# Performance work log

Hardware: AMD Instinct MI355X
Metric: run time of the kernel (lower is better)

The kernel has to match this reference:

```python
import jax, jax.numpy as jnp
import numpy as np
from jax import lax


def _conv(x, w, b, padding):
    # x: NCHW, w: OIHW
    out = lax.conv_general_dilated(x, w, (1, 1), padding,
                                   dimension_numbers=('NCHW', 'OIHW', 'NCHW'))
    return out + b[None, :, None, None]


def _bilinear_sample(img, ys, xs):
    # img: [B,C,H,W]; ys, xs: [B,N] absolute pixel coords; zero padding outside.
    B, C, H, W = img.shape
    y0 = jnp.floor(ys); x0 = jnp.floor(xs)
    wy1 = ys - y0; wy0 = 1.0 - wy1
    wx1 = xs - x0; wx0 = 1.0 - wx1
    img_flat = img.reshape(B, C, H * W)

    def corner(yc, xc, w):
        valid = (yc >= 0) & (yc <= H - 1) & (xc >= 0) & (xc <= W - 1)
        yi = jnp.clip(yc, 0, H - 1).astype(jnp.int32)
        xi = jnp.clip(xc, 0, W - 1).astype(jnp.int32)
        idx = yi * W + xi  # [B,N]
        g = jax.vmap(lambda im, i: im[:, i])(img_flat, idx)  # [B,C,N]
        return g * (w * valid.astype(img.dtype))[:, None, :]

    return (corner(y0, x0, wy0 * wx0) + corner(y0, x0 + 1, wy0 * wx1)
            + corner(y0 + 1, x0, wy1 * wx0) + corner(y0 + 1, x0 + 1, wy1 * wx1))


def setup_inputs() -> dict:
    key = jax.random.key(0)
    ks = jax.random.split(key, 20)
    B, C, Co, H, W = 8, 64, 64, 128, 128
    f = jnp.float32

    def w_init(k, shape):
        fan_in = int(np.prod(shape[1:]))
        return jax.random.normal(k, shape, dtype=f) * (1.0 / np.sqrt(fan_in))

    inp = {
        'x': jax.random.normal(ks[0], (B, C, H, W), dtype=f),
        'offset': jax.random.normal(ks[1], (B, 18, H, W), dtype=f),
        # STN localization
        'stn_w1': w_init(ks[2], (32, C, 7, 7)), 'stn_b1': jnp.zeros((32,), f),
        'stn_w2': w_init(ks[3], (64, 32, 5, 5)), 'stn_b2': jnp.zeros((64,), f),
        'fc_w': jax.random.normal(ks[4], (6, 64), dtype=f) * 0.01,
        'fc_b': jnp.array([1, 0, 0, 0, 1, 0], f) + jax.random.normal(ks[5], (6,), dtype=f) * 0.02,
        # DeformConv2d
        'dcn_w': w_init(ks[6], (C, C, 3, 3)), 'dcn_b': jnp.zeros((C,), f),
        # weight_gen 1x1
        'wg_w': w_init(ks[7], (2, 2 * C, 1, 1)), 'wg_b': jnp.zeros((2,), f),
        # ELK block
        'w3': w_init(ks[8], (Co, C, 3, 3)), 'b3': jnp.zeros((Co,), f),
        'w15': w_init(ks[9], (Co, C, 1, 5)), 'b15': jnp.zeros((Co,), f),
        'w51': w_init(ks[10], (Co, C, 5, 1)), 'b51': jnp.zeros((Co,), f),
        'w1': w_init(ks[11], (Co, 3 * Co, 1, 1)), 'b1': jnp.zeros((Co,), f),
    }
    return inp


def _forward(x, offset, stn_w1, stn_b1, stn_w2, stn_b2, fc_w, fc_b,
             dcn_w, dcn_b, wg_w, wg_b, w3, b3, w15, b15, w51, b51, w1, b1):
    B, C, H, W = x.shape

    # ---- STN ----
    h = jax.nn.relu(_conv(x, stn_w1, stn_b1, [(3, 3), (3, 3)]))
    h = lax.reduce_window(h, -jnp.inf, lax.max, (1, 1, 2, 2), (1, 1, 2, 2), 'VALID')
    h = jax.nn.relu(_conv(h, stn_w2, stn_b2, [(2, 2), (2, 2)]))
    feat = h.mean(axis=(2, 3))  # AdaptiveAvgPool2d(1) -> [B,64]
    theta = (feat @ fc_w.T + fc_b).reshape(B, 2, 3)

    # affine_grid, align_corners=False
    xs_n = (2.0 * jnp.arange(W, dtype=x.dtype) + 1.0) / W - 1.0
    ys_n = (2.0 * jnp.arange(H, dtype=x.dtype) + 1.0) / H - 1.0
    Xn, Yn = jnp.meshgrid(xs_n, ys_n, indexing='xy')  # [H,W]
    gx = theta[:, 0, 0, None, None] * Xn + theta[:, 0, 1, None, None] * Yn + theta[:, 0, 2, None, None]
    gy = theta[:, 1, 0, None, None] * Xn + theta[:, 1, 1, None, None] * Yn + theta[:, 1, 2, None, None]
    # grid_sample unnormalize, align_corners=False
    ix = ((gx + 1.0) * W - 1.0) * 0.5
    iy = ((gy + 1.0) * H - 1.0) * 0.5
    Fs = _bilinear_sample(x, iy.reshape(B, -1), ix.reshape(B, -1)).reshape(B, C, H, W)

    # ---- DeformConv2d(k=3, pad=1): offset layout [.., 2k]=dy, [.., 2k+1]=dx ----
    off = offset.reshape(B, 9, 2, H, W)
    ki = (jnp.arange(9, dtype=x.dtype) // 3) - 1.0  # kernel dy
    kj = (jnp.arange(9, dtype=x.dtype) % 3) - 1.0   # kernel dx
    Yb = jnp.arange(H, dtype=x.dtype)[:, None]
    Xb = jnp.arange(W, dtype=x.dtype)[None, :]
    sy = Yb[None, None] + ki[None, :, None, None] + off[:, :, 0]  # [B,9,H,W]
    sx = Xb[None, None] + kj[None, :, None, None] + off[:, :, 1]
    samp = _bilinear_sample(x, sy.reshape(B, -1), sx.reshape(B, -1)).reshape(B, C, 9, H, W)
    Fd = jnp.einsum('bckhw,ock->bohw', samp, dcn_w.reshape(C, C, 9)) + dcn_b[None, :, None, None]

    # ---- weighted fusion ----
    weights = jax.nn.softmax(_conv(jnp.concatenate([Fs, Fd], 1), wg_w, wg_b, [(0, 0), (0, 0)]), axis=1)
    fused = Fs * weights[:, 0:1] + Fd * weights[:, 1:2]

    # ---- ELK block ----
    o1 = _conv(fused, w3, b3, [(1, 1), (1, 1)])
    o2 = _conv(fused, w15, b15, [(0, 0), (2, 2)])
    o3 = _conv(fused, w51, b51, [(2, 2), (0, 0)])
    return _conv(jnp.concatenate([o1, o2, o3], 1), w1, b1, [(0, 0), (0, 0)])


def reference(x, offset, stn_w1, stn_b1, stn_w2, stn_b2, fc_w, fc_b,
              dcn_w, dcn_b, wg_w, wg_b, w3, b3, w15, b15, w51, b51, w1, b1):
    return _forward(x, offset, stn_w1, stn_b1, stn_w2, stn_b2, fc_w, fc_b,
                    dcn_w, dcn_b, wg_w, wg_b, w3, b3, w15, b15, w51, b51, w1, b1)
```

## Files before the change

### kernel.cpp

```cpp
#include <hip/hip_runtime.h>
#include <math.h>

#define Bn 8
#define Cn 64
#define Hn 128
#define Wn 128
#define HWn 16384

typedef __attribute__((ext_vector_type(8))) __bf16 bf16x8;
typedef __attribute__((ext_vector_type(4))) __bf16 bf16x4;
typedef __attribute__((ext_vector_type(4))) float f32x4;

__device__ __forceinline__ int xcd_swz(int bid, int chunk) {
  return (bid & 7) * chunk + (bid >> 3);
}

__global__ __launch_bounds__(256) void k_wprep(
    const float* __restrict__ stn_w1, const float* __restrict__ dcn_w,
    const float* __restrict__ w1, const float* __restrict__ w3,
    const float* __restrict__ w15, const float* __restrict__ w51,
    const float* __restrict__ stn_w2,
    const float* __restrict__ b3, const float* __restrict__ b15,
    const float* __restrict__ b51, const float* __restrict__ b1,
    __bf16* __restrict__ wfrag, __bf16* __restrict__ dcnD,
    __bf16* __restrict__ weffD, __bf16* __restrict__ w2frag,
    float* __restrict__ beff)
{
  int t = blockIdx.x * 256 + threadIdx.x;
  if (t < 100352) {
    int e = t & 7, l = (t >> 3) & 63, o16 = (t >> 9) & 1, ck = (t >> 10) & 1;
    int tap = t >> 11;
    int o = o16 * 16 + (l & 15), c = ck * 32 + (l >> 4) * 8 + e;
    wfrag[t] = (__bf16)stn_w1[(o * 64 + c) * 49 + tap];
    return;
  }
  t -= 100352;
  if (t < 36864) {
    int e = t & 7, l = (t >> 3) & 63, mf = (t >> 9) & 3, s = (t >> 11) & 1;
    int tap = t >> 12;
    int o = mf * 16 + (l & 15), c = s * 32 + (l >> 4) * 8 + e;
    dcnD[t] = (__bf16)dcn_w[(o * 64 + c) * 9 + tap];
    return;
  }
  t -= 36864;
  if (t < 53248) {
    const int DY[13] = {-2,-1,-1,-1, 0, 0, 0, 0, 0, 1, 1, 1, 2};
    const int DX[13] = { 0,-1, 0, 1,-2,-1, 0, 1, 2,-1, 0, 1, 0};
    int e = t & 7, l = (t >> 3) & 63, mf = (t >> 9) & 3, s = (t >> 11) & 1;
    int tap = t >> 12;
    int o = mf * 16 + (l & 15), c = s * 32 + (l >> 4) * 8 + e;
    int dy = DY[tap], dx = DX[tap];
    float v = 0.f;
    if (dy >= -1 && dy <= 1 && dx >= -1 && dx <= 1) {
      int k3 = (dy + 1) * 3 + (dx + 1);
      for (int m = 0; m < 64; m++) v = fmaf(w1[o * 192 + m], w3[(m * 64 + c) * 9 + k3], v);
    }
    if (dy == 0) {
      int k15 = dx + 2;
      for (int m = 0; m < 64; m++) v = fmaf(w1[o * 192 + 64 + m], w15[(m * 64 + c) * 5 + k15], v);
    }
    if (dx == 0) {
      int k51 = dy + 2;
      for (int m = 0; m < 64; m++) v = fmaf(w1[o * 192 + 128 + m], w51[(m * 64 + c) * 5 + k51], v);
    }
    weffD[t] = (__bf16)v;
    return;
  }
  t -= 53248;
  if (t < 51200) {
    int e = t & 7, l = (t >> 3) & 63, mf = (t >> 9) & 3;
    int tap = t >> 11;
    int o = mf * 16 + (l & 15), c = (l >> 4) * 8 + e;
    w2frag[t] = (__bf16)stn_w2[(o * 32 + c) * 25 + tap];
    return;
  }
  t -= 51200;
  if (t < 64) {
    float s = b1[t];
    for (int m = 0; m < 64; m++) {
      s = fmaf(w1[t * 192 + m],       b3[m],  s);
      s = fmaf(w1[t * 192 + 64 + m],  b15[m], s);
      s = fmaf(w1[t * 192 + 128 + m], b51[m], s);
    }
    beff[t] = s;
  }
}

__global__ __launch_bounds__(256) void k_xt(const float* __restrict__ x,
                                            __bf16* __restrict__ xT,
                                            __bf16* __restrict__ xC)
{
  int t = blockIdx.x * 256 + threadIdx.x;
  if (t >= 8 * 134 * 134 * 2) return;
  int half = t & 1;
  int p  = t >> 1;
  int wp = p % 134;
  int hp = (p / 134) % 134;
  int b  = p / (134 * 134);
  int h = hp - 3, w = wp - 3;
  bool inb = ((unsigned)h < 128u) && ((unsigned)w < 128u);
  const float* xb = x + (size_t)b * Cn * HWn + (size_t)(half * 32) * HWn + h * 128 + w;

  float v[32];
#pragma unroll
  for (int j = 0; j < 32; j++) v[j] = inb ? xb[(size_t)j * HWn] : 0.f;

  __bf16* dstT = xT + (size_t)p * 64 + half * 32;
#pragma unroll
  for (int g = 0; g < 4; g++) {
    bf16x8 r;
#pragma unroll
    for (int j = 0; j < 8; j++) r[j] = (__bf16)v[g * 8 + j];
    *(bf16x8*)(dstT + g * 8) = r;
    int oct = half * 4 + g;
    *(bf16x8*)(xC + ((((size_t)b * 8 + oct) * 134 + hp) * 144 + wp) * 8) = r;
  }
}

__global__ __launch_bounds__(256) void k_conv1m(
    const __bf16* __restrict__ xC, const __bf16* __restrict__ wfrag,
    const float* __restrict__ b1s, __bf16* __restrict__ t1T)
{
  __shared__ alignas(16) char tile[73728];
  const int lane = threadIdx.x & 63;
  const int wv   = threadIdx.x >> 6;
  const int swz  = xcd_swz(blockIdx.x, 64);
  const int b    = swz >> 6;
  const int h0   = (swz & 63) * 2;
  const int r    = wv >> 1;
  const int hf   = wv & 1;

  f32x4 acc[2][4];
#pragma unroll
  for (int o16 = 0; o16 < 2; o16++)
#pragma unroll
    for (int nf = 0; nf < 4; nf++) acc[o16][nf] = (f32x4){0.f, 0.f, 0.f, 0.f};

  const bf16x8* wf = (const bf16x8*)wfrag;
  const char* tb = (const char*)tile;
  const char* xCb = (const char*)xC;

  for (int ck = 0; ck < 2; ck++) {
    for (int i = wv; i < 72; i += 4) {
      int q = i / 18;
      int t = i - q * 18;
      const char* src = xCb
          + (((size_t)(b * 8 + ck * 4 + q) * 134 + h0) * 2304) + t * 1024 + lane * 16;
      char* dst = (char*)tile + i * 1024;
      __builtin_amdgcn_global_load_lds(
          (const __attribute__((address_space(1))) void*)src,
          (__attribute__((address_space(3))) void*)dst, 16, 0, 0);
    }
    __syncthreads();

    for (int tap = 0; tap < 49; tap++) {
      int dy7 = tap / 7;
      int dx7 = tap - dy7 * 7;
      bf16x8 a0 = wf[((tap * 2 + ck) * 2 + 0) * 64 + lane];
      bf16x8 a1 = wf[((tap * 2 + ck) * 2 + 1) * 64 + lane];
      const char* bp = tb + (lane >> 4) * 18432 + (r + dy7) * 2304
                          + (dx7 + hf * 64 + (lane & 15)) * 16;
#pragma unroll
      for (int nf = 0; nf < 4; nf++) {
        bf16x8 bv = *(const bf16x8*)(bp + nf * 256);
        acc[0][nf] = __builtin_amdgcn_mfma_f32_16x16x32_bf16(a0, bv, acc[0][nf], 0, 0, 0);
        acc[1][nf] = __builtin_amdgcn_mfma_f32_16x16x32_bf16(a1, bv, acc[1][nf], 0, 0, 0);
      }
    }
    __syncthreads();
  }

  int h = h0 + r;
#pragma unroll
  for (int o16 = 0; o16 < 2; o16++) {
    int ob = o16 * 16 + ((lane >> 4) << 2);
    float bb0 = b1s[ob], bb1 = b1s[ob + 1], bb2 = b1s[ob + 2], bb3 = b1s[ob + 3];
#pragma unroll
    for (int nf = 0; nf < 4; nf++) {
      int px = hf * 64 + nf * 16 + (lane & 15);
      bf16x4 rr;
      rr[0] = (__bf16)fmaxf(acc[o16][nf][0] + bb0, 0.f);
      rr[1] = (__bf16)fmaxf(acc[o16][nf][1] + bb1, 0.f);
      rr[2] = (__bf16)fmaxf(acc[o16][nf][2] + bb2, 0.f);
      rr[3] = (__bf16)fmaxf(acc[o16][nf][3] + bb3, 0.f);
      *(bf16x4*)(t1T + (((size_t)(b * 128 + h) * 128 + px)) * 32 + ob) = rr;
    }
  }
}

__global__ __launch_bounds__(256) void k_pool(const __bf16* __restrict__ t1T,
                                              __bf16* __restrict__ p1T)
{
  int id = blockIdx.x * 256 + threadIdx.x;
  if (id >= 8 * 68 * 68) return;
  int wp = id % 68, hp = (id / 68) % 68, b = id / (68 * 68);
  __bf16* dst = p1T + (size_t)id * 32;
  int ph = hp - 2, pw = wp - 2;
  if (((unsigned)ph >= 64u) || ((unsigned)pw >= 64u)) {
    bf16x8 z = {};
#pragma unroll
    for (int g = 0; g < 4; g++) *(bf16x8*)(dst + g * 8) = z;
    return;
  }
  const __bf16* s = t1T + (((size_t)(b * 128) + ph * 2) * 128 + pw * 2) * 32;
#pragma unroll
  for (int g = 0; g < 4; g++) {
    bf16x8 v0 = *(const bf16x8*)(s + g * 8);
    bf16x8 v1 = *(const bf16x8*)(s + 32 + g * 8);
    bf16x8 v2 = *(const bf16x8*)(s + 4096 + g * 8);
    bf16x8 v3 = *(const bf16x8*)(s + 4128 + g * 8);
    bf16x8 r;
#pragma unroll
    for (int j = 0; j < 8; j++) {
      float m = fmaxf(fmaxf((float)v0[j], (float)v1[j]),
                      fmaxf((float)v2[j], (float)v3[j]));
      r[j] = (__bf16)m;
    }
    *(bf16x8*)(dst + g * 8) = r;
  }
}

__global__ __launch_bounds__(256) void k_conv2m(
    const __bf16* __restrict__ p1T, const __bf16* __restrict__ w2frag,
    const float* __restrict__ b2s, float* __restrict__ t2)
{
  __shared__ alignas(16) char tile[34816];
  const int lane = threadIdx.x & 63;
  const int wv   = threadIdx.x >> 6;
  const int b    = blockIdx.x >> 4;
  const int h0   = (blockIdx.x & 15) * 4;

  f32x4 acc[4][4];
#pragma unroll
  for (int mf = 0; mf < 4; mf++)
#pragma unroll
    for (int nf = 0; nf < 4; nf++) acc[mf][nf] = (f32x4){0.f, 0.f, 0.f, 0.f};

  const char* src0 = (const char*)p1T + (((size_t)b * 68 + h0) * 68) * 64;
  for (int i = wv; i < 34; i += 4) {
    __builtin_amdgcn_global_load_lds(
        (const __attribute__((address_space(1))) void*)(src0 + i * 1024 + lane * 16),
        (__attribute__((address_space(3))) void*)((char*)tile + i * 1024), 16, 0, 0);
  }
  __syncthreads();

  const bf16x8* wf = (const bf16x8*)w2frag;
  const char* tb = (const char*)tile;
  for (int tap = 0; tap < 25; tap++) {
    int ky = tap / 5, kx = tap - ky * 5;
    bf16x8 a0 = wf[(tap * 4 + 0) * 64 + lane];
    bf16x8 a1 = wf[(tap * 4 + 1) * 64 + lane];
    bf16x8 a2 = wf[(tap * 4 + 2) * 64 + lane];
    bf16x8 a3 = wf[(tap * 4 + 3) * 64 + lane];
    const char* bp = tb + (((wv + ky) * 68 + kx + (lane & 15)) * 64) + (lane >> 4) * 16;
#pragma unroll
    for (int nf = 0; nf < 4; nf++) {
      bf16x8 bv = *(const bf16x8*)(bp + nf * 1024);
      acc[0][nf] = __builtin_amdgcn_mfma_f32_16x16x32_bf16(a0, bv, acc[0][nf], 0, 0, 0);
      acc[1][nf] = __builtin_amdgcn_mfma_f32_16x16x32_bf16(a1, bv, acc[1][nf], 0, 0, 0);
      acc[2][nf] = __builtin_amdgcn_mfma_f32_16x16x32_bf16(a2, bv, acc[2][nf], 0, 0, 0);
      acc[3][nf] = __builtin_amdgcn_mfma_f32_16x16x32_bf16(a3, bv, acc[3][nf], 0, 0, 0);
    }
  }

  int h = h0 + wv;
#pragma unroll
  for (int mf = 0; mf < 4; mf++) {
    int ob = mf * 16 + ((lane >> 4) << 2);
#pragma unroll
    for (int r = 0; r < 4; r++) {
      float bb = b2s[ob + r];
      float* orow = t2 + ((size_t)(b * 64 + ob + r)) * 4096 + h * 64 + (lane & 15);
#pragma unroll
      for (int nf = 0; nf < 4; nf++)
        orow[nf * 16] = fmaxf(acc[mf][nf][r] + bb, 0.f);
    }
  }
}

__global__ __launch_bounds__(256) void k_feat(const float* __restrict__ t2, float* __restrict__ feat)
{
  __shared__ float red[256];
  int bc = blockIdx.x;
  const float* s = t2 + (size_t)bc * 4096;
  float v = 0.f;
  for (int i = threadIdx.x; i < 4096; i += 256) v += s[i];
  red[threadIdx.x] = v;
  __syncthreads();
  for (int st = 128; st > 0; st >>= 1) {
    if (threadIdx.x < st) red[threadIdx.x] += red[threadIdx.x + st];
    __syncthreads();
  }
  if (threadIdx.x == 0) feat[bc] = red[0];
}

__global__ void k_theta(const float* __restrict__ feat, const float* __restrict__ fc_w,
                        const float* __restrict__ fc_b, float* __restrict__ theta)
{
  int tid = threadIdx.x;
  if (tid >= 48) return;
  int b = tid / 6, i = tid - b * 6;
  float s = 0.f;
  for (int k = 0; k < 64; k++) s = fmaf(feat[b * 64 + k], fc_w[i * 64 + k], s);
  theta[tid] = fmaf(s, 1.f / 4096.f, fc_b[i]);
}

__device__ __forceinline__ void bilin_setup(
    const __bf16* __restrict__ xb, float sy, float sx,
    const __bf16*& c00, const __bf16*& c01,
    const __bf16*& c10, const __bf16*& c11,
    float& w00, float& w01, float& w10, float& w11)
{
  float y0f = floorf(sy), x0f = floorf(sx);
  float wy1 = sy - y0f, wy0 = 1.f - wy1;
  float wx1 = sx - x0f, wx0 = 1.f - wx1;
  bool vy0 = (y0f >= 0.f) && (y0f <= 127.f);
  bool vy1 = (y0f >= -1.f) && (y0f <= 126.f);
  bool vx0 = (x0f >= 0.f) && (x0f <= 127.f);
  bool vx1 = (x0f >= -1.f) && (x0f <= 126.f);
  int yi0 = (int)fminf(fmaxf(y0f, 0.f), 127.f);
  int yi1 = (int)fminf(fmaxf(y0f + 1.f, 0.f), 127.f);
  int xi0 = (int)fminf(fmaxf(x0f, 0.f), 127.f);
  int xi1 = (int)fminf(fmaxf(x0f + 1.f, 0.f), 127.f);
  w00 = wy0 * wx0 * ((vy0 && vx0) ? 1.f : 0.f);
  w01 = wy0 * wx1 * ((vy0 && vx1) ? 1.f : 0.f);
  w10 = wy1 * wx0 * ((vy1 && vx0) ? 1.f : 0.f);
  w11 = wy1 * wx1 * ((vy1 && vx1) ? 1.f : 0.f);
  c00 = xb + ((size_t)((yi0 + 3) * 134) + xi0 + 3) * 64;
  c01 = xb + ((size_t)((yi0 + 3) * 134) + xi1 + 3) * 64;
  c10 = xb + ((size_t)((yi1 + 3) * 134) + xi0 + 3) * 64;
  c11 = xb + ((size_t)((yi1 + 3) * 134) + xi1 + 3) * 64;
}

__global__ __launch_bounds__(64) void k_dcnm(
    const __bf16* __restrict__ xT, const float* __restrict__ off,
    const float* __restrict__ theta,
    const __bf16* __restrict__ dcnD, const float* __restrict__ dcn_b,
    __bf16* __restrict__ FdT, __bf16* __restrict__ FsT)
{
  __shared__ alignas(16) char smem[2][2048];
  const int lane = threadIdx.x;
  const int swz  = xcd_swz(blockIdx.x, 1024);
  const int b    = swz >> 10;
  const int rem  = swz & 1023;
  const int h    = rem >> 3;
  const int px0  = (rem & 7) * 16;
  const int l15  = lane & 15;
  const int g    = lane >> 4;
  const int pg   = lane >> 2;
  const int q    = lane & 3;
  const int wg   = px0 + pg;

  const __bf16* xb = xT + (size_t)b * 134 * 134 * 64;

  const float* ob = off + (size_t)b * 18 * HWn + h * 128 + wg;
  float offs[18];
#pragma unroll
  for (int i = 0; i < 18; i++) offs[i] = ob[(size_t)i * HWn];

  {
    const float* t = theta + b * 6;
    float xn = (float)(2 * wg + 1) * (1.f / 128.f) - 1.f;
    float yn = (float)(2 * h + 1) * (1.f / 128.f) - 1.f;
    float gxv = t[0] * xn + t[1] * yn + t[2];
    float gyv = t[3] * xn + t[4] * yn + t[5];
    float ix = fmaf(gxv, 64.f, 63.5f);
    float iy = fmaf(gyv, 64.f, 63.5f);
    const __bf16 *c00, *c01, *c10, *c11;
    float w00, w01, w10, w11;
    bilin_setup(xb, iy, ix, c00, c01, c10, c11, w00, w01, w10, w11);
    __bf16* dst = FsT + ((size_t)b * HWn + h * 128 + wg) * 64;
#pragma unroll
    for (int s = 0; s < 2; s++) {
      int eo = q * 8 + s * 32;
      bf16x8 v00 = *(const bf16x8*)(c00 + eo);
      bf16x8 v01 = *(const bf16x8*)(c01 + eo);
      bf16x8 v10 = *(const bf16x8*)(c10 + eo);
      bf16x8 v11 = *(const bf16x8*)(c11 + eo);
      bf16x8 r;
#pragma unroll
      for (int j = 0; j < 8; j++) {
        float f = w00 * (float)v00[j] + w01 * (float)v01[j]
                + w10 * (float)v10[j] + w11 * (float)v11[j];
        r[j] = (__bf16)f;
      }
      *(bf16x8*)(dst + eo) = r;
    }
  }

  f32x4 acc[4];
#pragma unroll
  for (int mf = 0; mf < 4; mf++) acc[mf] = (f32x4){0.f, 0.f, 0.f, 0.f};
  const bf16x8* aD = (const bf16x8*)dcnD;

#pragma unroll
  for (int k = 0; k < 9; k++) {
    char* sm = smem[k & 1];
    float sy = (float)(h + k / 3 - 1) + offs[2 * k];
    float sx = (float)(wg + k % 3 - 1) + offs[2 * k + 1];
    const __bf16 *c00, *c01, *c10, *c11;
    float w00, w01, w10, w11;
    bilin_setup(xb, sy, sx, c00, c01, c10, c11, w00, w01, w10, w11);

#pragma unroll
    for (int s = 0; s < 2; s++) {
      int eo = q * 8 + s * 32;
      bf16x8 v00 = *(const bf16x8*)(c00 + eo);
      bf16x8 v01 = *(const bf16x8*)(c01 + eo);
      bf16x8 v10 = *(const bf16x8*)(c10 + eo);
      bf16x8 v11 = *(const bf16x8*)(c11 + eo);
      bf16x8 r;
#pragma unroll
      for (int j = 0; j < 8; j++) {
        float f = w00 * (float)v00[j] + w01 * (float)v01[j]
                + w10 * (float)v10[j] + w11 * (float)v11[j];
        r[j] = (__bf16)f;
      }
      int c = s * 4 + q;
      *(bf16x8*)(sm + pg * 128 + ((c ^ (pg & 7)) * 16)) = r;
    }

#pragma unroll
    for (int s = 0; s < 2; s++) {
      int c = s * 4 + g;
      bf16x8 a = *(const bf16x8*)(sm + l15 * 128 + ((c ^ (l15 & 7)) * 16));
      acc[0] = __builtin_amdgcn_mfma_f32_16x16x32_bf16(
          a, aD[((k * 2 + s) * 4 + 0) * 64 + lane], acc[0], 0, 0, 0);
      acc[1] = __builtin_amdgcn_mfma_f32_16x16x32_bf16(
          a, aD[((k * 2 + s) * 4 + 1) * 64 + lane], acc[1], 0, 0, 0);
      acc[2] = __builtin_amdgcn_mfma_f32_16x16x32_bf16(
          a, aD[((k * 2 + s) * 4 + 2) * 64 + lane], acc[2], 0, 0, 0);
      acc[3] = __builtin_amdgcn_mfma_f32_16x16x32_bf16(
          a, aD[((k * 2 + s) * 4 + 3) * 64 + lane], acc[3], 0, 0, 0);
    }
  }

  __bf16* fb = FdT + ((size_t)b * HWn + h * 128 + px0) * 64;
#pragma unroll
  for (int mf = 0; mf < 4; mf++) {
    int o = mf * 16 + l15;
    float bias = dcn_b[o];
#pragma unroll
    for (int r = 0; r < 4; r++) {
      int pxl = g * 4 + r;
      fb[(size_t)pxl * 64 + o] = (__bf16)(acc[mf][r] + bias);
    }
  }
}

#define FPL ((size_t)132 * 132 * 8)
__global__ __launch_bounds__(256) void k_fuseT(
    const __bf16* __restrict__ FsT, const __bf16* __restrict__ FdT,
    const float* __restrict__ wg_w, const float* __restrict__ wg_b,
    __bf16* __restrict__ fusedT)
{
  int id = blockIdx.x * 256 + threadIdx.x;
  if (id >= 8 * 132 * 132) return;
  int wp = id % 132;
  int hp = (id / 132) % 132;
  int b  = id / (132 * 132);
  size_t ppix = (size_t)(hp * 132 + wp) * 8;
  int h = hp - 2, w = wp - 2;
  if (((unsigned)h >= 128u) || ((unsigned)w >= 128u)) {
    bf16x8 z = {};
#pragma unroll
    for (int oct = 0; oct < 8; oct++)
      *(bf16x8*)(fusedT + ((size_t)b * 8 + oct) * FPL + ppix) = z;
    return;
  }
  const bf16x8* fs = (const bf16x8*)(FsT + ((size_t)b * HWn + h * 128 + w) * 64);
  const bf16x8* fd = (const bf16x8*)(FdT + ((size_t)b * HWn + h * 128 + w) * 64);
  bf16x8 fsv[8], fdv[8];
  float s0 = wg_b[0], s1 = wg_b[1];
#pragma unroll
  for (int oct = 0; oct < 8; oct++) {
    fsv[oct] = fs[oct];
    fdv[oct] = fd[oct];
#pragma unroll
    for (int j = 0; j < 8; j++) {
      int c = oct * 8 + j;
      float a = (float)fsv[oct][j], d = (float)fdv[oct][j];
      s0 = fmaf(wg_w[c],       a, fmaf(wg_w[64 + c],  d, s0));
      s1 = fmaf(wg_w[128 + c], a, fmaf(wg_w[192 + c], d, s1));
    }
  }
  float p0 = 1.f / (1.f + __expf(s1 - s0));
  float p1 = 1.f - p0;
#pragma unroll
  for (int oct = 0; oct < 8; oct++) {
    bf16x8 r;
#pragma unroll
    for (int j = 0; j < 8; j++)
      r[j] = (__bf16)(p0 * (float)fsv[oct][j] + p1 * (float)fdv[oct][j]);
    *(bf16x8*)(fusedT + ((size_t)b * 8 + oct) * FPL + ppix) = r;
  }
}

__global__ __launch_bounds__(256) void k_elkm(
    const __bf16* __restrict__ fusedT, const __bf16* __restrict__ weffD,
    const float* __restrict__ beff, float* __restrict__ out)
{
  const int DY[13] = {-2,-1,-1,-1, 0, 0, 0, 0, 0, 1, 1, 1, 2};
  const int DX[13] = { 0,-1, 0, 1,-2,-1, 0, 1, 2,-1, 0, 1, 0};
  const int lane = threadIdx.x & 63;
  const int wv   = threadIdx.x >> 6;
  const int swz  = xcd_swz(blockIdx.x, 64);
  const int b    = swz >> 6;
  const int h    = (swz & 63) * 2 + (wv >> 1);
  const int half = wv & 1;
  const int l15  = lane & 15;
  const int g    = lane >> 4;

  f32x4 acc[4][4];
#pragma unroll
  for (int mf = 0; mf < 4; mf++)
#pragma unroll
    for (int nf = 0; nf < 4; nf++) acc[mf][nf] = (f32x4){0.f, 0.f, 0.f, 0.f};

  const bf16x8* aD = (const bf16x8*)weffD;
  const __bf16* pl0 = fusedT + ((size_t)b * 8 + g) * FPL;
  const __bf16* pl1 = pl0 + 4 * FPL;

  for (int t = 0; t < 13; t++) {
    int hp = h + 2 + DY[t];
    size_t rowb = (size_t)(hp * 132 + half * 64 + 2 + DX[t] + l15) * 8;
#pragma unroll
    for (int s = 0; s < 2; s++) {
      const __bf16* pl = s ? pl1 : pl0;
      bf16x8 a0 = aD[((t * 2 + s) * 4 + 0) * 64 + lane];
      bf16x8 a1 = aD[((t * 2 + s) * 4 + 1) * 64 + lane];
      bf16x8 a2 = aD[((t * 2 + s) * 4 + 2) * 64 + lane];
      bf16x8 a3 = aD[((t * 2 + s) * 4 + 3) * 64 + lane];
#pragma unroll
      for (int nf = 0; nf < 4; nf++) {
        bf16x8 bv = *(const bf16x8*)(pl + rowb + (size_t)nf * 128);
        acc[0][nf] = __builtin_amdgcn_mfma_f32_16x16x32_bf16(a0, bv, acc[0][nf], 0, 0, 0);
        acc[1][nf] = __builtin_amdgcn_mfma_f32_16x16x32_bf16(a1, bv, acc[1][nf], 0, 0, 0);
        acc[2][nf] = __builtin_amdgcn_mfma_f32_16x16x32_bf16(a2, bv, acc[2][nf], 0, 0, 0);
        acc[3][nf] = __builtin_amdgcn_mfma_f32_16x16x32_bf16(a3, bv, acc[3][nf], 0, 0, 0);
      }
    }
  }

#pragma unroll
  for (int mf = 0; mf < 4; mf++) {
    int ob = mf * 16 + (g << 2);
#pragma unroll
    for (int r = 0; r < 4; r++) {
      int o = ob + r;
      float bb = beff[o];
      float* orow = out + ((size_t)(b * 64 + o)) * HWn + h * 128 + half * 64 + l15;
#pragma unroll
      for (int nf = 0; nf < 4; nf++)
        orow[nf * 16] = acc[mf][nf][r] + bb;
    }
  }
}

extern "C" void kernel_launch(void* const* d_in, const int* in_sizes, int n_in,
                              void* d_out, int out_size, void* d_ws, size_t ws_size,
                              hipStream_t stream)
{
  (void)in_sizes; (void)n_in; (void)out_size; (void)ws_size;
  const float* x      = (const float*)d_in[0];
  const float* offset = (const float*)d_in[1];
  const float* stn_w1 = (const float*)d_in[2];
  const float* stn_b1 = (const float*)d_in[3];
  const float* stn_w2 = (const float*)d_in[4];
  const float* stn_b2 = (const float*)d_in[5];
  const float* fc_w   = (const float*)d_in[6];
  const float* fc_b   = (const float*)d_in[7];
  const float* dcn_w  = (const float*)d_in[8];
  const float* dcn_b  = (const float*)d_in[9];
  const float* wg_w   = (const float*)d_in[10];
  const float* wg_b   = (const float*)d_in[11];
  const float* w3     = (const float*)d_in[12];
  const float* b3     = (const float*)d_in[13];
  const float* w15    = (const float*)d_in[14];
  const float* b15    = (const float*)d_in[15];
  const float* w51    = (const float*)d_in[16];
  const float* b51    = (const float*)d_in[17];
  const float* w1     = (const float*)d_in[18];
  const float* b1     = (const float*)d_in[19];

  float* ws      = (float*)d_ws;
  __bf16* xT     = (__bf16*)ws;
  __bf16* fusedT = (__bf16*)ws;
  __bf16* xC     = (__bf16*)(ws + 4596736);
  __bf16* FsT    = (__bf16*)(ws + 4596736);
  __bf16* t1T    = (__bf16*)(ws + 9536512);
  __bf16* FdT    = (__bf16*)(ws + 9536512);
  __bf16* p1T    = (__bf16*)(ws + 11633664);
  float*  t2     = ws + 12225536;
  float*  feat   = ws + 14322688;
  float*  theta  = ws + 14323200;
  __bf16* wfrag  = (__bf16*)(ws + 14323264);
  __bf16* w2frag = (__bf16*)(ws + 14373440);
  float*  beff   = ws + 14399040;
  __bf16* dcnD   = (__bf16*)(ws + 14399104);
  __bf16* weffD  = (__bf16*)(ws + 14417536);
  float*  out    = (float*)d_out;

  k_wprep <<<945,  256, 0, stream>>>(stn_w1, dcn_w, w1, w3, w15, w51, stn_w2,
                                     b3, b15, b51, b1,
                                     wfrag, dcnD, weffD, w2frag, beff);
  k_xt    <<<1123, 256, 0, stream>>>(x, xT, xC);
  k_conv1m<<<512,  256, 0, stream>>>(xC, wfrag, stn_b1, t1T);
  k_pool  <<<145,  256, 0, stream>>>(t1T, p1T);
  k_conv2m<<<128,  256, 0, stream>>>(p1T, w2frag, stn_b2, t2);
  k_feat  <<<512,  256, 0, stream>>>(t2, feat);
  k_theta <<<1,    64,  0, stream>>>(feat, fc_w, fc_b, theta);
  k_dcnm  <<<8192, 64,  0, stream>>>(xT, offset, theta, dcnD, dcn_b, FdT, FsT);
  k_fuseT <<<545,  256, 0, stream>>>(FsT, FdT, wg_w, wg_b, fusedT);
  k_elkm  <<<512,  256, 0, stream>>>(fusedT, weffD, beff, out);
}
```

Before: 192.0 us.

## Fuse maxpool into conv1 epilogue and spatial mean into conv2 epilogue

The 2x2 max-pool now runs inside the first STN conv kernel, which stages its output rows in shared memory and writes the pooled result straight into the padded p1T buffer. The zero border of p1T is now written by the weight-prep kernel. The second conv reduces its ReLU outputs to per-block partial channel sums instead of writing the full t2 tensor, and k_theta finishes the reduction. This removes the k_pool and k_feat launches and the t1T/t2 round trips through global memory, at the cost of extra LDS traffic and one more barrier in each conv epilogue.

```diff
diff --git a/kernel.cpp b/kernel.cpp
--- a/kernel.cpp
+++ b/kernel.cpp
@@ -24,7 +24,7 @@
     const float* __restrict__ b51, const float* __restrict__ b1,
     __bf16* __restrict__ wfrag, __bf16* __restrict__ dcnD,
     __bf16* __restrict__ weffD, __bf16* __restrict__ w2frag,
-    float* __restrict__ beff)
+    float* __restrict__ beff, __bf16* __restrict__ p1T)
 {
   int t = blockIdx.x * 256 + threadIdx.x;
   if (t < 100352) {
@@ -83,6 +83,13 @@
       s = fmaf(w1[t * 192 + 128 + m], b51[m], s);
     }
     beff[t] = s;
+    return;
+  }
+  t -= 64;
+  if (t < 73984) {
+    bf16x8 z = {};
+    *(bf16x8*)(p1T + (size_t)t * 16) = z;
+    *(bf16x8*)(p1T + (size_t)t * 16 + 8) = z;
   }
 }
 
@@ -119,7 +126,7 @@
 
 __global__ __launch_bounds__(256) void k_conv1m(
     const __bf16* __restrict__ xC, const __bf16* __restrict__ wfrag,
-    const float* __restrict__ b1s, __bf16* __restrict__ t1T)
+    const float* __restrict__ b1s, __bf16* __restrict__ p1T)
 {
   __shared__ alignas(16) char tile[73728];
   const int lane = threadIdx.x & 63;
@@ -129,6 +136,7 @@
   const int h0   = (swz & 63) * 2;
   const int r    = wv >> 1;
   const int hf   = wv & 1;
+  const int l15  = lane & 15;
 
   f32x4 acc[2][4];
 #pragma unroll
@@ -159,7 +167,7 @@
       bf16x8 a0 = wf[((tap * 2 + ck) * 2 + 0) * 64 + lane];
       bf16x8 a1 = wf[((tap * 2 + ck) * 2 + 1) * 64 + lane];
       const char* bp = tb + (lane >> 4) * 18432 + (r + dy7) * 2304
-                          + (dx7 + hf * 64 + (lane & 15)) * 16;
+                          + (dx7 + hf * 64 + l15) * 16;
 #pragma unroll
       for (int nf = 0; nf < 4; nf++) {
         bf16x8 bv = *(const bf16x8*)(bp + nf * 256);
@@ -170,65 +178,55 @@
     __syncthreads();
   }
 
-  int h = h0 + r;
 #pragma unroll
   for (int o16 = 0; o16 < 2; o16++) {
     int ob = o16 * 16 + ((lane >> 4) << 2);
     float bb0 = b1s[ob], bb1 = b1s[ob + 1], bb2 = b1s[ob + 2], bb3 = b1s[ob + 3];
 #pragma unroll
     for (int nf = 0; nf < 4; nf++) {
-      int px = hf * 64 + nf * 16 + (lane & 15);
+      int px = hf * 64 + nf * 16 + l15;
       bf16x4 rr;
       rr[0] = (__bf16)fmaxf(acc[o16][nf][0] + bb0, 0.f);
       rr[1] = (__bf16)fmaxf(acc[o16][nf][1] + bb1, 0.f);
       rr[2] = (__bf16)fmaxf(acc[o16][nf][2] + bb2, 0.f);
       rr[3] = (__bf16)fmaxf(acc[o16][nf][3] + bb3, 0.f);
-      *(bf16x4*)(t1T + (((size_t)(b * 128 + h) * 128 + px)) * 32 + ob) = rr;
-    }
-  }
-}
-
-__global__ __launch_bounds__(256) void k_pool(const __bf16* __restrict__ t1T,
-                                              __bf16* __restrict__ p1T)
-{
-  int id = blockIdx.x * 256 + threadIdx.x;
-  if (id >= 8 * 68 * 68) return;
-  int wp = id % 68, hp = (id / 68) % 68, b = id / (68 * 68);
-  __bf16* dst = p1T + (size_t)id * 32;
-  int ph = hp - 2, pw = wp - 2;
-  if (((unsigned)ph >= 64u) || ((unsigned)pw >= 64u)) {
-    bf16x8 z = {};
-#pragma unroll
-    for (int g = 0; g < 4; g++) *(bf16x8*)(dst + g * 8) = z;
-    return;
-  }
-  const __bf16* s = t1T + (((size_t)(b * 128) + ph * 2) * 128 + pw * 2) * 32;
-#pragma unroll
-  for (int g = 0; g < 4; g++) {
-    bf16x8 v0 = *(const bf16x8*)(s + g * 8);
-    bf16x8 v1 = *(const bf16x8*)(s + 32 + g * 8);
-    bf16x8 v2 = *(const bf16x8*)(s + 4096 + g * 8);
-    bf16x8 v3 = *(const bf16x8*)(s + 4128 + g * 8);
-    bf16x8 r;
+      *(bf16x4*)((char*)tile + (size_t)(r * 128 + px) * 64 + ob * 2) = rr;
+    }
+  }
+  __syncthreads();
+
+  {
+    int tid = threadIdx.x;
+    int wp = tid >> 2, cg = tid & 3;
+    const char* base = (const char*)tile;
+    bf16x8 v00 = *(const bf16x8*)(base + (size_t)(0 * 128 + 2 * wp) * 64 + cg * 16);
+    bf16x8 v01 = *(const bf16x8*)(base + (size_t)(0 * 128 + 2 * wp + 1) * 64 + cg * 16);
+    bf16x8 v10 = *(const bf16x8*)(base + (size_t)(1 * 128 + 2 * wp) * 64 + cg * 16);
+    bf16x8 v11 = *(const bf16x8*)(base + (size_t)(1 * 128 + 2 * wp + 1) * 64 + cg * 16);
+    bf16x8 rr;
 #pragma unroll
     for (int j = 0; j < 8; j++) {
-      float m = fmaxf(fmaxf((float)v0[j], (float)v1[j]),
-                      fmaxf((float)v2[j], (float)v3[j]));
-      r[j] = (__bf16)m;
-    }
-    *(bf16x8*)(dst + g * 8) = r;
+      float m = fmaxf(fmaxf((float)v00[j], (float)v01[j]),
+                      fmaxf((float)v10[j], (float)v11[j]));
+      rr[j] = (__bf16)m;
+    }
+    int hp = (swz & 63) + 2;
+    *(bf16x8*)(p1T + (((size_t)b * 68 + hp) * 68 + wp + 2) * 32 + cg * 8) = rr;
   }
 }
 
 __global__ __launch_bounds__(256) void k_conv2m(
     const __bf16* __restrict__ p1T, const __bf16* __restrict__ w2frag,
-    const float* __restrict__ b2s, float* __restrict__ t2)
+    const float* __restrict__ b2s, float* __restrict__ partial)
 {
   __shared__ alignas(16) char tile[34816];
+  __shared__ float sm2[4][16][64];
   const int lane = threadIdx.x & 63;
   const int wv   = threadIdx.x >> 6;
   const int b    = blockIdx.x >> 4;
-  const int h0   = (blockIdx.x & 15) * 4;
+  const int tl   = blockIdx.x & 15;
+  const int h0   = tl * 4;
+  const int l15  = lane & 15;
 
   f32x4 acc[4][4];
 #pragma unroll
@@ -252,7 +250,7 @@
     bf16x8 a1 = wf[(tap * 4 + 1) * 64 + lane];
     bf16x8 a2 = wf[(tap * 4 + 2) * 64 + lane];
     bf16x8 a3 = wf[(tap * 4 + 3) * 64 + lane];
-    const char* bp = tb + (((wv + ky) * 68 + kx + (lane & 15)) * 64) + (lane >> 4) * 16;
+    const char* bp = tb + (((wv + ky) * 68 + kx + l15) * 64) + (lane >> 4) * 16;
 #pragma unroll
     for (int nf = 0; nf < 4; nf++) {
       bf16x8 bv = *(const bf16x8*)(bp + nf * 1024);
@@ -263,46 +261,49 @@
     }
   }
 
-  int h = h0 + wv;
 #pragma unroll
   for (int mf = 0; mf < 4; mf++) {
     int ob = mf * 16 + ((lane >> 4) << 2);
 #pragma unroll
-    for (int r = 0; r < 4; r++) {
-      float bb = b2s[ob + r];
-      float* orow = t2 + ((size_t)(b * 64 + ob + r)) * 4096 + h * 64 + (lane & 15);
+    for (int rr = 0; rr < 4; rr++) {
+      float bb = b2s[ob + rr];
+      float s = 0.f;
 #pragma unroll
       for (int nf = 0; nf < 4; nf++)
-        orow[nf * 16] = fmaxf(acc[mf][nf][r] + bb, 0.f);
-    }
-  }
-}
-
-__global__ __launch_bounds__(256) void k_feat(const float* __restrict__ t2, float* __restrict__ feat)
-{
-  __shared__ float red[256];
-  int bc = blockIdx.x;
-  const float* s = t2 + (size_t)bc * 4096;
-  float v = 0.f;
-  for (int i = threadIdx.x; i < 4096; i += 256) v += s[i];
-  red[threadIdx.x] = v;
+        s += fmaxf(acc[mf][nf][rr] + bb, 0.f);
+      sm2[wv][l15][ob + rr] = s;
+    }
+  }
   __syncthreads();
-  for (int st = 128; st > 0; st >>= 1) {
-    if (threadIdx.x < st) red[threadIdx.x] += red[threadIdx.x + st];
-    __syncthreads();
-  }
-  if (threadIdx.x == 0) feat[bc] = red[0];
-}
-
-__global__ void k_theta(const float* __restrict__ feat, const float* __restrict__ fc_w,
-                        const float* __restrict__ fc_b, float* __restrict__ theta)
-{
+  if (threadIdx.x < 64) {
+    float s = 0.f;
+#pragma unroll
+    for (int w2 = 0; w2 < 4; w2++)
+      for (int l = 0; l < 16; l++) s += sm2[w2][l][threadIdx.x];
+    partial[(size_t)(b * 16 + tl) * 64 + threadIdx.x] = s;
+  }
+}
+
+__global__ __launch_bounds__(512) void k_theta(
+    const float* __restrict__ partial, const float* __restrict__ fc_w,
+    const float* __restrict__ fc_b, float* __restrict__ theta)
+{
+  __shared__ float featL[512];
   int tid = threadIdx.x;
-  if (tid >= 48) return;
-  int b = tid / 6, i = tid - b * 6;
-  float s = 0.f;
-  for (int k = 0; k < 64; k++) s = fmaf(feat[b * 64 + k], fc_w[i * 64 + k], s);
-  theta[tid] = fmaf(s, 1.f / 4096.f, fc_b[i]);
+  {
+    int b = tid >> 6, co = tid & 63;
+    float s = 0.f;
+#pragma unroll
+    for (int t = 0; t < 16; t++) s += partial[(size_t)(b * 16 + t) * 64 + co];
+    featL[tid] = s;
+  }
+  __syncthreads();
+  if (tid < 48) {
+    int b = tid / 6, i = tid - b * 6;
+    float s = 0.f;
+    for (int k = 0; k < 64; k++) s = fmaf(featL[b * 64 + k], fc_w[i * 64 + k], s);
+    theta[tid] = fmaf(s, 1.f / 4096.f, fc_b[i]);
+  }
 }
 
 __device__ __forceinline__ void bilin_setup(
@@ -588,11 +589,9 @@
   __bf16* fusedT = (__bf16*)ws;
   __bf16* xC     = (__bf16*)(ws + 4596736);
   __bf16* FsT    = (__bf16*)(ws + 4596736);
-  __bf16* t1T    = (__bf16*)(ws + 9536512);
   __bf16* FdT    = (__bf16*)(ws + 9536512);
   __bf16* p1T    = (__bf16*)(ws + 11633664);
-  float*  t2     = ws + 12225536;
-  float*  feat   = ws + 14322688;
+  float*  partial= ws + 12225536;
   float*  theta  = ws + 14323200;
   __bf16* wfrag  = (__bf16*)(ws + 14323264);
   __bf16* w2frag = (__bf16*)(ws + 14373440);
@@ -601,15 +600,13 @@
   __bf16* weffD  = (__bf16*)(ws + 14417536);
   float*  out    = (float*)d_out;
 
-  k_wprep <<<945,  256, 0, stream>>>(stn_w1, dcn_w, w1, w3, w15, w51, stn_w2,
+  k_wprep <<<1234, 256, 0, stream>>>(stn_w1, dcn_w, w1, w3, w15, w51, stn_w2,
                                      b3, b15, b51, b1,
-                                     wfrag, dcnD, weffD, w2frag, beff);
+                                     wfrag, dcnD, weffD, w2frag, beff, p1T);
   k_xt    <<<1123, 256, 0, stream>>>(x, xT, xC);
-  k_conv1m<<<512,  256, 0, stream>>>(xC, wfrag, stn_b1, t1T);
-  k_pool  <<<145,  256, 0, stream>>>(t1T, p1T);
-  k_conv2m<<<128,  256, 0, stream>>>(p1T, w2frag, stn_b2, t2);
-  k_feat  <<<512,  256, 0, stream>>>(t2, feat);
-  k_theta <<<1,    64,  0, stream>>>(feat, fc_w, fc_b, theta);
+  k_conv1m<<<512,  256, 0, stream>>>(xC, wfrag, stn_b1, p1T);
+  k_conv2m<<<128,  256, 0, stream>>>(p1T, w2frag, stn_b2, partial);
+  k_theta <<<1,    512, 0, stream>>>(partial, fc_w, fc_b, theta);
   k_dcnm  <<<8192, 64,  0, stream>>>(xT, offset, theta, dcnD, dcn_b, FdT, FsT);
   k_fuseT <<<545,  256, 0, stream>>>(FsT, FdT, wg_w, wg_b, fusedT);
   k_elkm  <<<512,  256, 0, stream>>>(fusedT, weffD, beff, out);
```

Result: faster. 179.0 us (-6.8%).
